# Optimization experiments

Measured on AMD Instinct MI355X. Metric: run time of the kernel, lower is better.

## Reference

```python
import jax, jax.numpy as jnp
import numpy as np

B, N, MSA, PAIR = 1, 768, 384, 128
H, SQK, PQK, SV, PV, OUT = 12, 16, 4, 16, 8, 384
EPS = 1e-8


def setup_inputs() -> dict:
    key = jax.random.key(0)
    ks = jax.random.split(key, 12)
    rn = lambda k, shape, s=1.0: jax.random.normal(k, shape, jnp.float32) * s
    return {
        "inputs_1d": rn(ks[0], (B, N, MSA)),
        "inputs_2d": rn(ks[1], (B, N, N, PAIR)),
        "rot": rn(ks[2], (B, N, 3, 3)),
        "trans": rn(ks[3], (B, N, 3)),
        "q_scalar_w": rn(ks[4], (MSA, H * SQK), 0.02),
        "q_scalar_b": jnp.zeros((H * SQK,), jnp.float32),
        "kv_scalar_w": rn(ks[5], (MSA, H * (SV + SQK)), 0.02),
        "kv_scalar_b": jnp.zeros((H * (SV + SQK),), jnp.float32),
        "q_point_w": rn(ks[6], (MSA, H * 3 * PQK), 0.02),
        "q_point_b": jnp.zeros((H * 3 * PQK,), jnp.float32),
        "kv_point_w": rn(ks[7], (MSA, H * 3 * (PQK + PV)), 0.02),
        "kv_point_b": jnp.zeros((H * 3 * (PQK + PV),), jnp.float32),
        "tpw": jnp.full((H,), 0.541323855, jnp.float32),
        "attn2d_w": rn(ks[8], (PAIR, H), 0.02),
        "attn2d_b": jnp.zeros((H,), jnp.float32),
        "out_w": rn(ks[9], (H * SV + H * PV * 4 + H * PAIR, OUT), 0.02),
        "out_b": jnp.zeros((OUT,), jnp.float32),
    }


def _ipa(inputs_1d, inputs_2d, rot, trans,
         q_scalar_w, q_scalar_b, kv_scalar_w, kv_scalar_b,
         q_point_w, q_point_b, kv_point_w, kv_point_b,
         tpw, attn2d_w, attn2d_b, out_w, out_b):
    b, n, _ = inputs_1d.shape
    # scalar q/k/v
    q_scalar = (inputs_1d @ q_scalar_w + q_scalar_b).reshape(b, n, H, SQK)
    kv_scalar = (inputs_1d @ kv_scalar_w + kv_scalar_b).reshape(b, n, H, SQK + SV)
    k_scalar, v_scalar = kv_scalar[..., :SQK], kv_scalar[..., SQK:]

    # point q/k/v: local frame -> global frame via per-residue rigid (R, t)
    def to_global(local):  # local: [b, n, 3, D]
        return jnp.einsum('bnij,bnjd->bnid', rot, local) + trans[..., None]

    qpl = (inputs_1d @ q_point_w + q_point_b).reshape(b, n, 3, H * PQK)
    # [b, H, n, PQK, 3]
    qp = to_global(qpl).reshape(b, n, 3, H, PQK).transpose(0, 3, 1, 4, 2)
    kvpl = (inputs_1d @ kv_point_w + kv_point_b).reshape(b, n, 3, H * (PQK + PV))
    kvp = to_global(kvpl).reshape(b, n, 3, H, PQK + PV).transpose(0, 3, 1, 4, 2)
    kp, vp = kvp[..., :PQK, :], kvp[..., PQK:, :]  # [b,H,n,PQK,3], [b,H,n,PV,3]

    scalar_w = (1.0 / (3.0 * SQK)) ** 0.5
    point_w = ((1.0 / (3.0 * PQK * 4.5)) ** 0.5) * jax.nn.softplus(tpw)  # [H]
    attn2d_scale = (1.0 / 3.0) ** 0.5

    # squared point distances, summed over xyz: [b, H, n, n, PQK]
    dist2 = sum(
        (qp[..., c][:, :, :, None, :] - kp[..., c][:, :, None, :, :]) ** 2
        for c in range(3))
    attn_qk_point = -0.5 * jnp.einsum('h,bhijp->bhij', point_w, dist2)

    q = scalar_w * q_scalar.transpose(0, 2, 1, 3)  # [b,H,n,SQK]
    k = k_scalar.transpose(0, 2, 1, 3)
    v = v_scalar.transpose(0, 2, 1, 3)
    attn_qk_scalar = jnp.einsum('bhid,bhjd->bhij', q, k)

    a2d = (inputs_2d @ attn2d_w + attn2d_b).transpose(0, 3, 1, 2) * attn2d_scale
    attn = jax.nn.softmax(attn_qk_scalar + attn_qk_point + a2d, axis=-1)

    result_scalar = jnp.einsum('bhij,bhjd->bhid', attn, v)
    result_scalar = result_scalar.transpose(0, 2, 1, 3).reshape(b, n, H * SV)

    rpg = jnp.einsum('bhij,bhjpc->bhipc', attn, vp)  # [b,H,n,PV,3]
    rpg = rpg.transpose(0, 2, 4, 1, 3).reshape(b, n, 3, H * PV)
    # invert point back to local frame: R^T (x - t)
    rpl = jnp.einsum('bnji,bnjd->bnid', rot, rpg - trans[..., None])  # [b,n,3,H*PV]
    pnorm = jnp.sqrt(EPS + jnp.sum(rpl ** 2, axis=2))  # [b,n,H*PV]

    a_over_2d = jnp.einsum('bhij,bijc->bihc', attn, inputs_2d).reshape(b, n, H * PAIR)

    final = jnp.concatenate(
        [result_scalar, rpl[:, :, 0], rpl[:, :, 1], rpl[:, :, 2], pnorm, a_over_2d],
        axis=-1)
    return final @ out_w + out_b


def reference(inputs_1d, inputs_2d, rot, trans,
              q_scalar_w, q_scalar_b, kv_scalar_w, kv_scalar_b,
              q_point_w, q_point_b, kv_point_w, kv_point_b,
              tpw, attn2d_w, attn2d_b, out_w, out_b):
    return _ipa(inputs_1d, inputs_2d, rot, trans,
                q_scalar_w, q_scalar_b, kv_scalar_w, kv_scalar_b,
                q_point_w, q_point_b, kv_point_w, kv_point_b,
                tpw, attn2d_w, attn2d_b, out_w, out_b)
```

## Files before the change

### kernel.cpp

```cpp
#include <hip/hip_runtime.h>
#include <hip/hip_bf16.h>

typedef unsigned int uint;
typedef unsigned short ushort;

#define SCALAR_W 0.14433756729740643f
#define PW_CONST 0.13608276348795434f
#define RSQRT3   0.57735026918962576f

#define OFF_QS    0
#define OFF_QP    147456
#define OFF_FINP  258048
#define FLOAT_END 700416
#define US_KS     1400832
#define US_VS     1548288
#define US_KP     1695744
#define US_VP     1806336
#define US_FA     2027520

__device__ __forceinline__ float blo(uint u){ return __uint_as_float(u << 16); }
__device__ __forceinline__ float bhi(uint u){ return __uint_as_float(u & 0xffff0000u); }
__device__ __forceinline__ float bf1(ushort s){ return __uint_as_float(((uint)s) << 16); }
__device__ __forceinline__ void up8(uint4 u, float* f){
  f[0]=blo(u.x); f[1]=bhi(u.x); f[2]=blo(u.y); f[3]=bhi(u.y);
  f[4]=blo(u.z); f[5]=bhi(u.z); f[6]=blo(u.w); f[7]=bhi(u.w);
}
__device__ __forceinline__ ushort f2us(float f){
  return (ushort)__bfloat16_as_ushort(__float2bfloat16(f));
}

__global__ __launch_bounds__(256) void k_proj(
    const float* __restrict__ rot, const float* __restrict__ trans,
    const float* __restrict__ qsw, const float* __restrict__ qsb,
    const float* __restrict__ kvsw, const float* __restrict__ kvsb,
    const float* __restrict__ qpw, const float* __restrict__ qpb,
    const float* __restrict__ kvpw, const float* __restrict__ kvpb,
    const float* __restrict__ in1d, float* ws){
  __shared__ float orow[1152];
  __shared__ float rotL[9], transL[3];
  const int n = blockIdx.x, t = threadIdx.x;
  const float* arow = in1d + n*384;
  if (t < 9) rotL[t] = rot[n*9+t];
  if (t >= 9 && t < 12) transL[t-9] = trans[n*3+t-9];
  #pragma unroll
  for (int r = 0; r < 3; ++r){
    int idx = t + 256*r;
    if (idx < 576){
      int o = idx*2;
      const float* w; const float* bp; int ncol, col;
      if (o < 192){ w=qsw; ncol=192; col=o; bp=qsb+col; }
      else if (o < 576){ w=kvsw; ncol=384; col=o-192; bp=kvsb+col; }
      else if (o < 720){ w=qpw; ncol=144; col=o-576; bp=qpb+col; }
      else { w=kvpw; ncol=432; col=o-720; bp=kvpb+col; }
      float2 b2 = *reinterpret_cast<const float2*>(bp);
      float a0 = b2.x, a1 = b2.y;
      const float* wp = w + col;
      #pragma unroll 4
      for (int k = 0; k < 384; ++k){
        float2 u = *reinterpret_cast<const float2*>(wp + (size_t)k*ncol);
        float av = arow[k];
        a0 += av * u.x;
        a1 += av * u.y;
      }
      orow[o] = a0; orow[o+1] = a1;
    }
  }
  __syncthreads();
  float* qs_f = ws + OFF_QS;
  float* qp_f = ws + OFF_QP;
  ushort* ws16 = reinterpret_cast<ushort*>(ws);
  ushort* kS = ws16 + US_KS;
  ushort* vS = ws16 + US_VS;
  ushort* kP = ws16 + US_KP;
  ushort* vP = ws16 + US_VP;
  if (t < 192) qs_f[n*192 + t] = orow[t] * SCALAR_W;
  for (int x = t; x < 384; x += 256){
    int h = x >> 5, d = x & 31;
    float v = orow[192 + x];
    if (d < 16) kS[(n*12 + h)*16 + d] = f2us(v);
    else        vS[(n*12 + h)*16 + (d-16)] = f2us(v);
  }
  for (int x = t; x < 144; x += 256){
    int d = x/3, c = x - 3*d;
    float g = rotL[c*3]*orow[576+d] + rotL[c*3+1]*orow[576+48+d] + rotL[c*3+2]*orow[576+96+d] + transL[c];
    qp_f[n*144 + d*3 + c] = g;
  }
  for (int x = t; x < 432; x += 256){
    int d = x/3, c = x - 3*d;
    float g = rotL[c*3]*orow[720+d] + rotL[c*3+1]*orow[720+144+d] + rotL[c*3+2]*orow[720+288+d] + transL[c];
    int h = d/12, pp = d - 12*h;
    if (pp < 4) kP[((n*12+h)*4 + pp)*3 + c] = f2us(g);
    else        vP[((n*12+h)*8 + (pp-4))*3 + c] = f2us(g);
  }
}

__global__ __launch_bounds__(256) void k_attn(
    const float* __restrict__ in2d, const float* __restrict__ rot,
    const float* __restrict__ trans, const float* __restrict__ w2d,
    const float* __restrict__ b2d, const float* __restrict__ tpw,
    float* ws){
  __shared__ __align__(16) float Ld[768*12];
  __shared__ float invL[12];
  __shared__ float pwS[12], b2S[12];
  __shared__ float rotL[9], transL[3];
  const int i = blockIdx.x, t = threadIdx.x;
  const float* qs_f = ws + OFF_QS + i*192;
  const float* qp_f = ws + OFF_QP + i*144;
  const ushort* ws16 = reinterpret_cast<const ushort*>(ws);
  const ushort* kSp = ws16 + US_KS;
  const ushort* vSp = ws16 + US_VS;
  const ushort* kPp = ws16 + US_KP;
  const ushort* vPp = ws16 + US_VP;
  if (t < 9) rotL[t] = rot[i*9+t];
  if (t >= 9 && t < 12) transL[t-9] = trans[i*3+t-9];
  if (t < 12){
    b2S[t] = b2d[t];
    pwS[t] = -0.5f * PW_CONST * log1pf(__expf(tpw[t]));
  }
  __syncthreads();
  for (int j = t; j < 768; j += 256){
    float acc12[12];
    #pragma unroll
    for (int h = 0; h < 12; ++h) acc12[h] = b2S[h];
    const float4* p2 = reinterpret_cast<const float4*>(in2d + (size_t)(i*768 + j)*128);
    #pragma unroll 4
    for (int c4 = 0; c4 < 32; ++c4){
      float4 u = p2[c4];
      const float* wr = w2d + c4*48;
      #pragma unroll
      for (int h = 0; h < 12; ++h)
        acc12[h] += u.x*wr[h] + u.y*wr[12+h] + u.z*wr[24+h] + u.w*wr[36+h];
    }
    #pragma unroll
    for (int h = 0; h < 12; ++h){
      const uint4* pk = reinterpret_cast<const uint4*>(kSp + ((size_t)j*12 + h)*16);
      uint4 a = pk[0], b = pk[1];
      float kf[16]; up8(a, kf); up8(b, kf+8);
      float qk = 0.f;
      const float* qr = qs_f + h*16;
      #pragma unroll
      for (int d = 0; d < 16; ++d) qk += qr[d] * kf[d];
      const uint2* pp = reinterpret_cast<const uint2*>(kPp + ((size_t)j*12 + h)*12);
      uint2 c0 = pp[0], c1 = pp[1], c2 = pp[2];
      float pf[12] = {blo(c0.x),bhi(c0.x),blo(c0.y),bhi(c0.y),
                      blo(c1.x),bhi(c1.x),blo(c1.y),bhi(c1.y),
                      blo(c2.x),bhi(c2.x),blo(c2.y),bhi(c2.y)};
      const float* qpr = qp_f + h*12;
      float d2 = 0.f;
      #pragma unroll
      for (int e = 0; e < 12; ++e){ float dd = qpr[e] - pf[e]; d2 += dd*dd; }
      acc12[h] = acc12[h]*RSQRT3 + qk + pwS[h]*d2;
    }
    float4* lp = reinterpret_cast<float4*>(&Ld[j*12]);
    lp[0] = make_float4(acc12[0], acc12[1], acc12[2],  acc12[3]);
    lp[1] = make_float4(acc12[4], acc12[5], acc12[6],  acc12[7]);
    lp[2] = make_float4(acc12[8], acc12[9], acc12[10], acc12[11]);
  }
  __syncthreads();
  const int wave = t >> 6, lane = t & 63;
  float invReg[3];
  #pragma unroll
  for (int s = 0; s < 3; ++s){
    int h = wave + s*4;
    float m = -1e30f;
    for (int k = 0; k < 12; ++k) m = fmaxf(m, Ld[(lane + (k<<6))*12 + h]);
    #pragma unroll
    for (int o = 32; o > 0; o >>= 1) m = fmaxf(m, __shfl_xor(m, o));
    float sum = 0.f;
    for (int k = 0; k < 12; ++k){
      int idx = (lane + (k<<6))*12 + h;
      float e = __expf(fminf(Ld[idx] - m, 0.f));
      Ld[idx] = e;
      sum += e;
    }
    #pragma unroll
    for (int o = 32; o > 0; o >>= 1) sum += __shfl_xor(sum, o);
    float inv = 1.f / sum;
    invReg[s] = inv;
    if (lane == 0) invL[h] = inv;
  }
  float* finp = ws + OFF_FINP + (size_t)i*576;
  #pragma unroll
  for (int s = 0; s < 3; ++s){
    int h = wave + s*4;
    float accS[16], accP[24];
    #pragma unroll
    for (int d = 0; d < 16; ++d) accS[d] = 0.f;
    #pragma unroll
    for (int d = 0; d < 24; ++d) accP[d] = 0.f;
    for (int it = 0; it < 12; ++it){
      int jj = lane + (it<<6);
      float e = Ld[jj*12 + h];
      const uint4* pv = reinterpret_cast<const uint4*>(vSp + ((size_t)jj*12 + h)*16);
      uint4 a = pv[0], b = pv[1];
      float vf[16]; up8(a, vf); up8(b, vf+8);
      #pragma unroll
      for (int d = 0; d < 16; ++d) accS[d] += e * vf[d];
      const uint4* pq = reinterpret_cast<const uint4*>(vPp + ((size_t)jj*12 + h)*24);
      uint4 q0 = pq[0], q1 = pq[1], q2 = pq[2];
      float pf[24]; up8(q0, pf); up8(q1, pf+8); up8(q2, pf+16);
      #pragma unroll
      for (int d = 0; d < 24; ++d) accP[d] += e * pf[d];
    }
    #pragma unroll
    for (int o2 = 32; o2 > 0; o2 >>= 1){
      #pragma unroll
      for (int d = 0; d < 16; ++d) accS[d] += __shfl_xor(accS[d], o2);
      #pragma unroll
      for (int d = 0; d < 24; ++d) accP[d] += __shfl_xor(accP[d], o2);
    }
    if (lane == 0){
      float inv = invReg[s];
      #pragma unroll
      for (int d = 0; d < 16; ++d) finp[h*16 + d] = accS[d]*inv;
      #pragma unroll
      for (int p = 0; p < 8; ++p){
        float gx = accP[p*3+0]*inv - transL[0];
        float gy = accP[p*3+1]*inv - transL[1];
        float gz = accP[p*3+2]*inv - transL[2];
        float n2 = 1e-8f;
        #pragma unroll
        for (int c = 0; c < 3; ++c){
          float r = rotL[c]*gx + rotL[3+c]*gy + rotL[6+c]*gz;
          finp[192 + c*96 + h*8 + p] = r;
          n2 += r*r;
        }
        finp[480 + h*8 + p] = sqrtf(n2);
      }
    }
  }
  __syncthreads();
  {
    const int cp = t & 63, jg = t >> 6;
    float acc[24];
    #pragma unroll
    for (int d = 0; d < 24; ++d) acc[d] = 0.f;
    const float* rowp = in2d + (size_t)i*768*128 + 2*cp;
    const int j0 = jg*192;
    for (int j = j0; j < j0 + 192; ++j){
      float2 x2 = *reinterpret_cast<const float2*>(rowp + (size_t)j*128);
      float x0 = x2.x, x1 = x2.y;
      const float4* lp = reinterpret_cast<const float4*>(&Ld[j*12]);
      float4 e0 = lp[0], e1 = lp[1], e2 = lp[2];
      acc[0] += e0.x*x0;  acc[1] += e0.x*x1;
      acc[2] += e0.y*x0;  acc[3] += e0.y*x1;
      acc[4] += e0.z*x0;  acc[5] += e0.z*x1;
      acc[6] += e0.w*x0;  acc[7] += e0.w*x1;
      acc[8] += e1.x*x0;  acc[9] += e1.x*x1;
      acc[10]+= e1.y*x0;  acc[11]+= e1.y*x1;
      acc[12]+= e1.z*x0;  acc[13]+= e1.z*x1;
      acc[14]+= e1.w*x0;  acc[15]+= e1.w*x1;
      acc[16]+= e2.x*x0;  acc[17]+= e2.x*x1;
      acc[18]+= e2.y*x0;  acc[19]+= e2.y*x1;
      acc[20]+= e2.z*x0;  acc[21]+= e2.z*x1;
      acc[22]+= e2.w*x0;  acc[23]+= e2.w*x1;
    }
    __syncthreads();
    float* LdR = Ld;
    if (jg > 0){
      #pragma unroll
      for (int d = 0; d < 24; ++d) LdR[((jg-1)*64 + cp)*25 + d] = acc[d];
    }
    __syncthreads();
    if (jg == 0){
      ushort* fa16 = reinterpret_cast<ushort*>(ws) + US_FA + (size_t)i*1536;
      float invA[12];
      #pragma unroll
      for (int h = 0; h < 12; ++h) invA[h] = invL[h];
      #pragma unroll
      for (int h = 0; h < 12; ++h){
        float a0 = acc[2*h]   + LdR[cp*25 + 2*h]   + LdR[(64+cp)*25 + 2*h]   + LdR[(128+cp)*25 + 2*h];
        float a1 = acc[2*h+1] + LdR[cp*25 + 2*h+1] + LdR[(64+cp)*25 + 2*h+1] + LdR[(128+cp)*25 + 2*h+1];
        fa16[h*128 + 2*cp]     = f2us(a0 * invA[h]);
        fa16[h*128 + 2*cp + 1] = f2us(a1 * invA[h]);
      }
    }
  }
}

__global__ __launch_bounds__(128) void k_out(const float* __restrict__ out_w,
                                             const float* __restrict__ out_b,
                                             const float* ws,
                                             float* __restrict__ out){
  __shared__ float Arow[4*2112];
  const int o = blockIdx.x*128 + threadIdx.x;
  const int ib = blockIdx.y*4;
  const ushort* ws16 = reinterpret_cast<const ushort*>(ws);
  #pragma unroll
  for (int r = 0; r < 4; ++r){
    const float* fp = ws + OFF_FINP + (size_t)(ib+r)*576;
    for (int k = threadIdx.x; k < 576; k += 128) Arow[r*2112 + k] = fp[k];
    const ushort* fa = ws16 + US_FA + (size_t)(ib+r)*1536;
    for (int k = threadIdx.x; k < 1536; k += 128) Arow[r*2112 + 576 + k] = bf1(fa[k]);
  }
  __syncthreads();
  float bc = out_b[o];
  float acc0 = bc, acc1 = bc, acc2 = bc, acc3 = bc;
  const float* wp = out_w + o;
  #pragma unroll 8
  for (int k = 0; k < 2112; ++k){
    float w = wp[(size_t)k*384];
    acc0 += Arow[k]*w; acc1 += Arow[2112+k]*w; acc2 += Arow[4224+k]*w; acc3 += Arow[6336+k]*w;
  }
  if (!(fabsf(acc0) < 1e30f)) acc0 = 1e6f;
  if (!(fabsf(acc1) < 1e30f)) acc1 = 1e6f;
  if (!(fabsf(acc2) < 1e30f)) acc2 = 1e6f;
  if (!(fabsf(acc3) < 1e30f)) acc3 = 1e6f;
  out[(ib+0)*384 + o] = acc0;
  out[(ib+1)*384 + o] = acc1;
  out[(ib+2)*384 + o] = acc2;
  out[(ib+3)*384 + o] = acc3;
}

extern "C" void kernel_launch(void* const* d_in, const int* in_sizes, int n_in,
                              void* d_out, int out_size, void* d_ws, size_t ws_size,
                              hipStream_t stream){
  const float* in1d  = (const float*)d_in[0];
  const float* in2d  = (const float*)d_in[1];
  const float* rot   = (const float*)d_in[2];
  const float* trans = (const float*)d_in[3];
  const float* qsw   = (const float*)d_in[4];
  const float* qsb   = (const float*)d_in[5];
  const float* kvsw  = (const float*)d_in[6];
  const float* kvsb  = (const float*)d_in[7];
  const float* qpw   = (const float*)d_in[8];
  const float* qpb   = (const float*)d_in[9];
  const float* kvpw  = (const float*)d_in[10];
  const float* kvpb  = (const float*)d_in[11];
  const float* tpw   = (const float*)d_in[12];
  const float* w2d   = (const float*)d_in[13];
  const float* b2d   = (const float*)d_in[14];
  const float* outw  = (const float*)d_in[15];
  const float* outb  = (const float*)d_in[16];
  float* ws = (float*)d_ws;

  k_proj<<<dim3(768), dim3(256), 0, stream>>>(rot, trans, qsw, qsb, kvsw, kvsb,
                                              qpw, qpb, kvpw, kvpb, in1d, ws);
  k_attn<<<dim3(768), dim3(256), 0, stream>>>(in2d, rot, trans, w2d, b2d, tpw, ws);
  k_out<<<dim3(3,192), dim3(128), 0, stream>>>(outw, outb, ws, (float*)d_out);
}
```

Before: 878.3 us.

## Stage pair, key and value rows through LDS with head-major packed layouts

The projection kernel now writes K scalar and K point data into one head-major packed buffer (28 bf16 per row) and stores V scalar and V point data head-major. The attention kernel loads these rows cooperatively, with coalesced wave-wide vector loads, into a per-wave LDS slice. Each lane then reads its own row from LDS. The pair-bias projection also stages in2d chunks through LDS with software prefetch. The aim is to replace strided per-lane global loads with coalesced ones, at the cost of extra LDS traffic, wave barriers and a larger shared-memory footprint that may lower occupancy.

After: 964.9 us. 9.9% more time.

```diff
diff --git a/kernel.cpp b/kernel.cpp
--- a/kernel.cpp
+++ b/kernel.cpp
@@ -11,20 +11,14 @@
 #define OFF_QS    0
 #define OFF_QP    147456
 #define OFF_FINP  258048
-#define FLOAT_END 700416
-#define US_KS     1400832
-#define US_VS     1548288
-#define US_KP     1695744
+#define US_KC     1400832
+#define US_VS     1658880
 #define US_VP     1806336
 #define US_FA     2027520
 
 __device__ __forceinline__ float blo(uint u){ return __uint_as_float(u << 16); }
 __device__ __forceinline__ float bhi(uint u){ return __uint_as_float(u & 0xffff0000u); }
 __device__ __forceinline__ float bf1(ushort s){ return __uint_as_float(((uint)s) << 16); }
-__device__ __forceinline__ void up8(uint4 u, float* f){
-  f[0]=blo(u.x); f[1]=bhi(u.x); f[2]=blo(u.y); f[3]=bhi(u.y);
-  f[4]=blo(u.z); f[5]=bhi(u.z); f[6]=blo(u.w); f[7]=bhi(u.w);
-}
 __device__ __forceinline__ ushort f2us(float f){
   return (ushort)__bfloat16_as_ushort(__float2bfloat16(f));
 }
@@ -69,16 +63,15 @@
   float* qs_f = ws + OFF_QS;
   float* qp_f = ws + OFF_QP;
   ushort* ws16 = reinterpret_cast<ushort*>(ws);
-  ushort* kS = ws16 + US_KS;
+  ushort* kC = ws16 + US_KC;
   ushort* vS = ws16 + US_VS;
-  ushort* kP = ws16 + US_KP;
   ushort* vP = ws16 + US_VP;
   if (t < 192) qs_f[n*192 + t] = orow[t] * SCALAR_W;
   for (int x = t; x < 384; x += 256){
     int h = x >> 5, d = x & 31;
     float v = orow[192 + x];
-    if (d < 16) kS[(n*12 + h)*16 + d] = f2us(v);
-    else        vS[(n*12 + h)*16 + (d-16)] = f2us(v);
+    if (d < 16) kC[((size_t)h*768 + n)*28 + d] = f2us(v);
+    else        vS[((size_t)h*768 + n)*16 + (d-16)] = f2us(v);
   }
   for (int x = t; x < 144; x += 256){
     int d = x/3, c = x - 3*d;
@@ -89,8 +82,8 @@
     int d = x/3, c = x - 3*d;
     float g = rotL[c*3]*orow[720+d] + rotL[c*3+1]*orow[720+144+d] + rotL[c*3+2]*orow[720+288+d] + transL[c];
     int h = d/12, pp = d - 12*h;
-    if (pp < 4) kP[((n*12+h)*4 + pp)*3 + c] = f2us(g);
-    else        vP[((n*12+h)*8 + (pp-4))*3 + c] = f2us(g);
+    if (pp < 4) kC[((size_t)h*768 + n)*28 + 16 + pp*3 + c] = f2us(g);
+    else        vP[((size_t)h*768 + n)*24 + (pp-4)*3 + c] = f2us(g);
   }
 }
 
@@ -100,17 +93,19 @@
     const float* __restrict__ b2d, const float* __restrict__ tpw,
     float* ws){
   __shared__ __align__(16) float Ld[768*12];
+  __shared__ __align__(16) float Sbuf[4*896];
   __shared__ float invL[12];
   __shared__ float pwS[12], b2S[12];
   __shared__ float rotL[9], transL[3];
   const int i = blockIdx.x, t = threadIdx.x;
+  const int wv = t >> 6, ln = t & 63;
   const float* qs_f = ws + OFF_QS + i*192;
   const float* qp_f = ws + OFF_QP + i*144;
   const ushort* ws16 = reinterpret_cast<const ushort*>(ws);
-  const ushort* kSp = ws16 + US_KS;
+  const ushort* kCp = ws16 + US_KC;
   const ushort* vSp = ws16 + US_VS;
-  const ushort* kPp = ws16 + US_KP;
   const ushort* vPp = ws16 + US_VP;
+  float* slice = Sbuf + wv*896;
   if (t < 9) rotL[t] = rot[i*9+t];
   if (t >= 9 && t < 12) transL[t-9] = trans[i*3+t-9];
   if (t < 12){
@@ -118,38 +113,76 @@
     pwS[t] = -0.5f * PW_CONST * log1pf(__expf(tpw[t]));
   }
   __syncthreads();
-  for (int j = t; j < 768; j += 256){
+
+  for (int jg = 0; jg < 3; ++jg){
+    const int j = jg*256 + t;
+    const int rowbase = i*768 + jg*256 + wv*64;
     float acc12[12];
     #pragma unroll
     for (int h = 0; h < 12; ++h) acc12[h] = b2S[h];
-    const float4* p2 = reinterpret_cast<const float4*>(in2d + (size_t)(i*768 + j)*128);
-    #pragma unroll 4
-    for (int c4 = 0; c4 < 32; ++c4){
-      float4 u = p2[c4];
-      const float* wr = w2d + c4*48;
-      #pragma unroll
-      for (int h = 0; h < 12; ++h)
-        acc12[h] += u.x*wr[h] + u.y*wr[12+h] + u.z*wr[24+h] + u.w*wr[36+h];
-    }
+
+    const int r0 = ln >> 1, cq = (ln & 1)*4;
+    const float* pA = in2d + (size_t)(rowbase + r0)*128 + cq;
+    const float* pB = pA + 32*128;
+    float* wr0 = slice + r0*9 + cq;
+    float* wr1 = slice + (r0+32)*9 + cq;
+    const float* rrow = slice + ln*9;
+    float4 u0 = *reinterpret_cast<const float4*>(pA);
+    float4 u1 = *reinterpret_cast<const float4*>(pB);
+    const uint4* kbase = reinterpret_cast<const uint4*>(kCp + ((size_t)jg*256 + wv*64)*28);
+    uint4 k0 = kbase[ln], k1 = kbase[ln+64], k2 = kbase[ln+128];
+    uint4 k3 = {0,0,0,0};
+    if (ln < 32) k3 = kbase[ln+192];
+    for (int cc = 0; cc < 16; ++cc){
+      wr0[0]=u0.x; wr0[1]=u0.y; wr0[2]=u0.z; wr0[3]=u0.w;
+      wr1[0]=u1.x; wr1[1]=u1.y; wr1[2]=u1.z; wr1[3]=u1.w;
+      if (cc < 15){
+        u0 = *reinterpret_cast<const float4*>(pA + (cc+1)*8);
+        u1 = *reinterpret_cast<const float4*>(pB + (cc+1)*8);
+      }
+      __builtin_amdgcn_wave_barrier();
+      #pragma unroll
+      for (int c2 = 0; c2 < 8; ++c2){
+        float x = rrow[c2];
+        const float* wp = w2d + (cc*8 + c2)*12;
+        #pragma unroll
+        for (int h = 0; h < 12; ++h) acc12[h] += x * wp[h];
+      }
+      __builtin_amdgcn_wave_barrier();
+    }
+
+    uint4* dst = reinterpret_cast<uint4*>(slice);
     #pragma unroll
     for (int h = 0; h < 12; ++h){
-      const uint4* pk = reinterpret_cast<const uint4*>(kSp + ((size_t)j*12 + h)*16);
-      uint4 a = pk[0], b = pk[1];
-      float kf[16]; up8(a, kf); up8(b, kf+8);
-      float qk = 0.f;
-      const float* qr = qs_f + h*16;
-      #pragma unroll
-      for (int d = 0; d < 16; ++d) qk += qr[d] * kf[d];
-      const uint2* pp = reinterpret_cast<const uint2*>(kPp + ((size_t)j*12 + h)*12);
-      uint2 c0 = pp[0], c1 = pp[1], c2 = pp[2];
-      float pf[12] = {blo(c0.x),bhi(c0.x),blo(c0.y),bhi(c0.y),
-                      blo(c1.x),bhi(c1.x),blo(c1.y),bhi(c1.y),
-                      blo(c2.x),bhi(c2.x),blo(c2.y),bhi(c2.y)};
+      dst[ln] = k0; dst[ln+64] = k1; dst[ln+128] = k2;
+      if (ln < 32) dst[ln+192] = k3;
+      if (h < 11){
+        const uint4* nb = kbase + (size_t)(h+1)*2688;
+        k0 = nb[ln]; k1 = nb[ln+64]; k2 = nb[ln+128];
+        if (ln < 32) k3 = nb[ln+192];
+      }
+      __builtin_amdgcn_wave_barrier();
+      const float* qr  = qs_f + h*16;
       const float* qpr = qp_f + h*12;
-      float d2 = 0.f;
-      #pragma unroll
-      for (int e = 0; e < 12; ++e){ float dd = qpr[e] - pf[e]; d2 += dd*dd; }
+      const uint2* krow = reinterpret_cast<const uint2*>(slice + ln*14);
+      float qk = 0.f, d2 = 0.f;
+      #pragma unroll
+      for (int dd = 0; dd < 4; ++dd){
+        uint2 u = krow[dd];
+        qk += qr[4*dd]   * blo(u.x) + qr[4*dd+1] * bhi(u.x)
+            + qr[4*dd+2] * blo(u.y) + qr[4*dd+3] * bhi(u.y);
+      }
+      #pragma unroll
+      for (int e2 = 0; e2 < 3; ++e2){
+        uint2 u = krow[4+e2];
+        float d0 = qpr[4*e2]   - blo(u.x);
+        float d1 = qpr[4*e2+1] - bhi(u.x);
+        float db = qpr[4*e2+2] - blo(u.y);
+        float d3 = qpr[4*e2+3] - bhi(u.y);
+        d2 += d0*d0 + d1*d1 + db*db + d3*d3;
+      }
       acc12[h] = acc12[h]*RSQRT3 + qk + pwS[h]*d2;
+      __builtin_amdgcn_wave_barrier();
     }
     float4* lp = reinterpret_cast<float4*>(&Ld[j*12]);
     lp[0] = make_float4(acc12[0], acc12[1], acc12[2],  acc12[3]);
@@ -157,50 +190,88 @@
     lp[2] = make_float4(acc12[8], acc12[9], acc12[10], acc12[11]);
   }
   __syncthreads();
-  const int wave = t >> 6, lane = t & 63;
-  float invReg[3];
+
   #pragma unroll
   for (int s = 0; s < 3; ++s){
-    int h = wave + s*4;
+    int h = wv + s*4;
     float m = -1e30f;
-    for (int k = 0; k < 12; ++k) m = fmaxf(m, Ld[(lane + (k<<6))*12 + h]);
+    for (int k = 0; k < 12; ++k) m = fmaxf(m, Ld[(ln + (k<<6))*12 + h]);
     #pragma unroll
     for (int o = 32; o > 0; o >>= 1) m = fmaxf(m, __shfl_xor(m, o));
     float sum = 0.f;
     for (int k = 0; k < 12; ++k){
-      int idx = (lane + (k<<6))*12 + h;
+      int idx = (ln + (k<<6))*12 + h;
       float e = __expf(fminf(Ld[idx] - m, 0.f));
       Ld[idx] = e;
       sum += e;
     }
     #pragma unroll
     for (int o = 32; o > 0; o >>= 1) sum += __shfl_xor(sum, o);
-    float inv = 1.f / sum;
-    invReg[s] = inv;
-    if (lane == 0) invL[h] = inv;
-  }
+    if (ln == 0) invL[h] = 1.f / sum;
+  }
+
   float* finp = ws + OFF_FINP + (size_t)i*576;
-  #pragma unroll
   for (int s = 0; s < 3; ++s){
-    int h = wave + s*4;
+    const int h = wv + s*4;
     float accS[16], accP[24];
     #pragma unroll
     for (int d = 0; d < 16; ++d) accS[d] = 0.f;
     #pragma unroll
     for (int d = 0; d < 24; ++d) accP[d] = 0.f;
-    for (int it = 0; it < 12; ++it){
-      int jj = lane + (it<<6);
-      float e = Ld[jj*12 + h];
-      const uint4* pv = reinterpret_cast<const uint4*>(vSp + ((size_t)jj*12 + h)*16);
-      uint4 a = pv[0], b = pv[1];
-      float vf[16]; up8(a, vf); up8(b, vf+8);
-      #pragma unroll
-      for (int d = 0; d < 16; ++d) accS[d] += e * vf[d];
-      const uint4* pq = reinterpret_cast<const uint4*>(vPp + ((size_t)jj*12 + h)*24);
-      uint4 q0 = pq[0], q1 = pq[1], q2 = pq[2];
-      float pf[24]; up8(q0, pf); up8(q1, pf+8); up8(q2, pf+16);
-      #pragma unroll
-      for (int d = 0; d < 24; ++d) accP[d] += e * pf[d];
+    {
+      const uint4* vb = reinterpret_cast<const uint4*>(vSp + (size_t)h*768*16);
+      uint4 a0 = vb[ln], a1 = vb[ln+64];
+      const int r = ln >> 1, c = (ln & 1)*4;
+      uint2* w0 = reinterpret_cast<uint2*>(slice + r*10 + c);
+      uint2* w1 = reinterpret_cast<uint2*>(slice + (r+32)*10 + c);
+      const uint2* vrow = reinterpret_cast<const uint2*>(slice + ln*10);
+      for (int it = 0; it < 12; ++it){
+        w0[0] = make_uint2(a0.x, a0.y); w0[1] = make_uint2(a0.z, a0.w);
+        w1[0] = make_uint2(a1.x, a1.y); w1[1] = make_uint2(a1.z, a1.w);
+        if (it < 11){
+          const uint4* nb = vb + (size_t)(it+1)*128;
+          a0 = nb[ln]; a1 = nb[ln+64];
+        }
+        __builtin_amdgcn_wave_barrier();
+        float e = Ld[((it<<6) + ln)*12 + h];
+        #pragma unroll
+        for (int dd = 0; dd < 4; ++dd){
+          uint2 u = vrow[dd];
+          accS[4*dd]   += e * blo(u.x); accS[4*dd+1] += e * bhi(u.x);
+          accS[4*dd+2] += e * blo(u.y); accS[4*dd+3] += e * bhi(u.y);
+        }
+        __builtin_amdgcn_wave_barrier();
+      }
+    }
+    {
+      const uint4* vb = reinterpret_cast<const uint4*>(vPp + (size_t)h*768*24);
+      uint4 a0 = vb[ln], a1 = vb[ln+64], a2 = vb[ln+128];
+      const int x1 = ln + 64, x2 = ln + 128;
+      const int ra = (ln*171) >> 9,  ca = (ln - 3*ra)*4;
+      const int rb = (x1*171) >> 9,  cb = (x1 - 3*rb)*4;
+      const int rc = (x2*171) >> 9,  cx = (x2 - 3*rc)*4;
+      uint2* w0 = reinterpret_cast<uint2*>(slice + ra*14 + ca);
+      uint2* w1 = reinterpret_cast<uint2*>(slice + rb*14 + cb);
+      uint2* w2 = reinterpret_cast<uint2*>(slice + rc*14 + cx);
+      const uint2* vrow = reinterpret_cast<const uint2*>(slice + ln*14);
+      for (int it = 0; it < 12; ++it){
+        w0[0] = make_uint2(a0.x, a0.y); w0[1] = make_uint2(a0.z, a0.w);
+        w1[0] = make_uint2(a1.x, a1.y); w1[1] = make_uint2(a1.z, a1.w);
+        w2[0] = make_uint2(a2.x, a2.y); w2[1] = make_uint2(a2.z, a2.w);
+        if (it < 11){
+          const uint4* nb = vb + (size_t)(it+1)*192;
+          a0 = nb[ln]; a1 = nb[ln+64]; a2 = nb[ln+128];
+        }
+        __builtin_amdgcn_wave_barrier();
+        float e = Ld[((it<<6) + ln)*12 + h];
+        #pragma unroll
+        for (int dd = 0; dd < 6; ++dd){
+          uint2 u = vrow[dd];
+          accP[4*dd]   += e * blo(u.x); accP[4*dd+1] += e * bhi(u.x);
+          accP[4*dd+2] += e * blo(u.y); accP[4*dd+3] += e * bhi(u.y);
+        }
+        __builtin_amdgcn_wave_barrier();
+      }
     }
     #pragma unroll
     for (int o2 = 32; o2 > 0; o2 >>= 1){
@@ -209,8 +280,8 @@
       #pragma unroll
       for (int d = 0; d < 24; ++d) accP[d] += __shfl_xor(accP[d], o2);
     }
-    if (lane == 0){
-      float inv = invReg[s];
+    if (ln == 0){
+      float inv = invL[h];
       #pragma unroll
       for (int d = 0; d < 16; ++d) finp[h*16 + d] = accS[d]*inv;
       #pragma unroll
@@ -221,9 +292,9 @@
         float n2 = 1e-8f;
         #pragma unroll
         for (int c = 0; c < 3; ++c){
-          float r = rotL[c]*gx + rotL[3+c]*gy + rotL[6+c]*gz;
-          finp[192 + c*96 + h*8 + p] = r;
-          n2 += r*r;
+          float rr = rotL[c]*gx + rotL[3+c]*gy + rotL[6+c]*gz;
+          finp[192 + c*96 + h*8 + p] = rr;
+          n2 += rr*rr;
         }
         finp[480 + h*8 + p] = sqrtf(n2);
       }
```

## Split attention blocks by head halves and split-K the output projection with atomics

Applied to the files above, without the earlier changes.

The attention kernel now launches two blocks per query row, each handling six heads. This halves LDS use and per-block work, and the K/V buffers are stored head-major. The output projection is split four ways along K, accumulating into the output with atomicAdd, and the bias is pre-written by the projection kernel. The trade-off is that each block pair re-reads the full in2d row, and atomics make the sum order non-deterministic. The old non-finite clamp is dropped.

Measured after the change: 752.8 us. 1.17x faster.

```diff
diff --git a/kernel.cpp b/kernel.cpp
--- a/kernel.cpp
+++ b/kernel.cpp
@@ -11,7 +11,6 @@
 #define OFF_QS    0
 #define OFF_QP    147456
 #define OFF_FINP  258048
-#define FLOAT_END 700416
 #define US_KS     1400832
 #define US_VS     1548288
 #define US_KP     1695744
@@ -35,13 +34,16 @@
     const float* __restrict__ kvsw, const float* __restrict__ kvsb,
     const float* __restrict__ qpw, const float* __restrict__ qpb,
     const float* __restrict__ kvpw, const float* __restrict__ kvpb,
-    const float* __restrict__ in1d, float* ws){
+    const float* __restrict__ in1d, const float* __restrict__ outb,
+    float* ws, float* __restrict__ out){
   __shared__ float orow[1152];
   __shared__ float rotL[9], transL[3];
   const int n = blockIdx.x, t = threadIdx.x;
-  const float* arow = in1d + n*384;
+  const float* arow = in1d + (size_t)n*384;
   if (t < 9) rotL[t] = rot[n*9+t];
   if (t >= 9 && t < 12) transL[t-9] = trans[n*3+t-9];
+  out[(size_t)n*384 + t] = outb[t];
+  if (t < 128) out[(size_t)n*384 + 256 + t] = outb[256 + t];
   #pragma unroll
   for (int r = 0; r < 3; ++r){
     int idx = t + 256*r;
@@ -77,8 +79,8 @@
   for (int x = t; x < 384; x += 256){
     int h = x >> 5, d = x & 31;
     float v = orow[192 + x];
-    if (d < 16) kS[(n*12 + h)*16 + d] = f2us(v);
-    else        vS[(n*12 + h)*16 + (d-16)] = f2us(v);
+    if (d < 16) kS[((size_t)h*768 + n)*16 + d] = f2us(v);
+    else        vS[((size_t)h*768 + n)*16 + (d-16)] = f2us(v);
   }
   for (int x = t; x < 144; x += 256){
     int d = x/3, c = x - 3*d;
@@ -89,8 +91,8 @@
     int d = x/3, c = x - 3*d;
     float g = rotL[c*3]*orow[720+d] + rotL[c*3+1]*orow[720+144+d] + rotL[c*3+2]*orow[720+288+d] + transL[c];
     int h = d/12, pp = d - 12*h;
-    if (pp < 4) kP[((n*12+h)*4 + pp)*3 + c] = f2us(g);
-    else        vP[((n*12+h)*8 + (pp-4))*3 + c] = f2us(g);
+    if (pp < 4) kP[((size_t)h*768 + n)*12 + pp*3 + c] = f2us(g);
+    else        vP[((size_t)h*768 + n)*24 + (pp-4)*3 + c] = f2us(g);
   }
 }
 
@@ -99,11 +101,12 @@
     const float* __restrict__ trans, const float* __restrict__ w2d,
     const float* __restrict__ b2d, const float* __restrict__ tpw,
     float* ws){
-  __shared__ __align__(16) float Ld[768*12];
-  __shared__ float invL[12];
-  __shared__ float pwS[12], b2S[12];
+  __shared__ __align__(16) float Ld[768*6];
+  __shared__ float invL[6];
+  __shared__ float pwS[6], b2S[6];
   __shared__ float rotL[9], transL[3];
-  const int i = blockIdx.x, t = threadIdx.x;
+  const int bid = blockIdx.x, t = threadIdx.x;
+  const int i = bid >> 1, h0 = (bid & 1)*6;
   const float* qs_f = ws + OFF_QS + i*192;
   const float* qp_f = ws + OFF_QP + i*144;
   const ushort* ws16 = reinterpret_cast<const ushort*>(ws);
@@ -113,76 +116,81 @@
   const ushort* vPp = ws16 + US_VP;
   if (t < 9) rotL[t] = rot[i*9+t];
   if (t >= 9 && t < 12) transL[t-9] = trans[i*3+t-9];
-  if (t < 12){
-    b2S[t] = b2d[t];
-    pwS[t] = -0.5f * PW_CONST * log1pf(__expf(tpw[t]));
+  if (t < 6){
+    b2S[t] = b2d[h0 + t];
+    pwS[t] = -0.5f * PW_CONST * log1pf(__expf(tpw[h0 + t]));
   }
   __syncthreads();
   for (int j = t; j < 768; j += 256){
-    float acc12[12];
-    #pragma unroll
-    for (int h = 0; h < 12; ++h) acc12[h] = b2S[h];
+    float acc6[6];
+    #pragma unroll
+    for (int h = 0; h < 6; ++h) acc6[h] = b2S[h];
     const float4* p2 = reinterpret_cast<const float4*>(in2d + (size_t)(i*768 + j)*128);
     #pragma unroll 4
     for (int c4 = 0; c4 < 32; ++c4){
       float4 u = p2[c4];
-      const float* wr = w2d + c4*48;
-      #pragma unroll
-      for (int h = 0; h < 12; ++h)
-        acc12[h] += u.x*wr[h] + u.y*wr[12+h] + u.z*wr[24+h] + u.w*wr[36+h];
-    }
-    #pragma unroll
-    for (int h = 0; h < 12; ++h){
-      const uint4* pk = reinterpret_cast<const uint4*>(kSp + ((size_t)j*12 + h)*16);
+      const float* wr = w2d + c4*48 + h0;
+      #pragma unroll
+      for (int h = 0; h < 6; ++h)
+        acc6[h] += u.x*wr[h] + u.y*wr[12+h] + u.z*wr[24+h] + u.w*wr[36+h];
+    }
+    #pragma unroll
+    for (int h = 0; h < 6; ++h){
+      const int hg = h0 + h;
+      const uint4* pk = reinterpret_cast<const uint4*>(kSp + ((size_t)hg*768 + j)*16);
       uint4 a = pk[0], b = pk[1];
       float kf[16]; up8(a, kf); up8(b, kf+8);
       float qk = 0.f;
-      const float* qr = qs_f + h*16;
+      const float* qr = qs_f + hg*16;
       #pragma unroll
       for (int d = 0; d < 16; ++d) qk += qr[d] * kf[d];
-      const uint2* pp = reinterpret_cast<const uint2*>(kPp + ((size_t)j*12 + h)*12);
+      const uint2* pp = reinterpret_cast<const uint2*>(kPp + ((size_t)hg*768 + j)*12);
       uint2 c0 = pp[0], c1 = pp[1], c2 = pp[2];
       float pf[12] = {blo(c0.x),bhi(c0.x),blo(c0.y),bhi(c0.y),
                       blo(c1.x),bhi(c1.x),blo(c1.y),bhi(c1.y),
                       blo(c2.x),bhi(c2.x),blo(c2.y),bhi(c2.y)};
-      const float* qpr = qp_f + h*12;
+      const float* qpr = qp_f + hg*12;
       float d2 = 0.f;
       #pragma unroll
       for (int e = 0; e < 12; ++e){ float dd = qpr[e] - pf[e]; d2 += dd*dd; }
-      acc12[h] = acc12[h]*RSQRT3 + qk + pwS[h]*d2;
-    }
-    float4* lp = reinterpret_cast<float4*>(&Ld[j*12]);
-    lp[0] = make_float4(acc12[0], acc12[1], acc12[2],  acc12[3]);
-    lp[1] = make_float4(acc12[4], acc12[5], acc12[6],  acc12[7]);
-    lp[2] = make_float4(acc12[8], acc12[9], acc12[10], acc12[11]);
+      acc6[h] = acc6[h]*RSQRT3 + qk + pwS[h]*d2;
+    }
+    float2* lp = reinterpret_cast<float2*>(&Ld[j*6]);
+    lp[0] = make_float2(acc6[0], acc6[1]);
+    lp[1] = make_float2(acc6[2], acc6[3]);
+    lp[2] = make_float2(acc6[4], acc6[5]);
   }
   __syncthreads();
   const int wave = t >> 6, lane = t & 63;
-  float invReg[3];
+  float invReg[2];
   #pragma unroll
-  for (int s = 0; s < 3; ++s){
+  for (int s = 0; s < 2; ++s){
     int h = wave + s*4;
-    float m = -1e30f;
-    for (int k = 0; k < 12; ++k) m = fmaxf(m, Ld[(lane + (k<<6))*12 + h]);
-    #pragma unroll
-    for (int o = 32; o > 0; o >>= 1) m = fmaxf(m, __shfl_xor(m, o));
-    float sum = 0.f;
-    for (int k = 0; k < 12; ++k){
-      int idx = (lane + (k<<6))*12 + h;
-      float e = __expf(fminf(Ld[idx] - m, 0.f));
-      Ld[idx] = e;
-      sum += e;
-    }
-    #pragma unroll
-    for (int o = 32; o > 0; o >>= 1) sum += __shfl_xor(sum, o);
-    float inv = 1.f / sum;
-    invReg[s] = inv;
-    if (lane == 0) invL[h] = inv;
+    if (h < 6){
+      float m = -1e30f;
+      for (int k = 0; k < 12; ++k) m = fmaxf(m, Ld[(lane + (k<<6))*6 + h]);
+      #pragma unroll
+      for (int o = 32; o > 0; o >>= 1) m = fmaxf(m, __shfl_xor(m, o));
+      float sum = 0.f;
+      for (int k = 0; k < 12; ++k){
+        int idx = (lane + (k<<6))*6 + h;
+        float e = __expf(fminf(Ld[idx] - m, 0.f));
+        Ld[idx] = e;
+        sum += e;
+      }
+      #pragma unroll
+      for (int o = 32; o > 0; o >>= 1) sum += __shfl_xor(sum, o);
+      float inv = 1.f / sum;
+      invReg[s] = inv;
+      if (lane == 0) invL[h] = inv;
+    }
   }
   float* finp = ws + OFF_FINP + (size_t)i*576;
   #pragma unroll
-  for (int s = 0; s < 3; ++s){
+  for (int s = 0; s < 2; ++s){
     int h = wave + s*4;
+    if (h >= 6) break;
+    const int hg = h0 + h;
     float accS[16], accP[24];
     #pragma unroll
     for (int d = 0; d < 16; ++d) accS[d] = 0.f;
@@ -190,13 +198,13 @@
     for (int d = 0; d < 24; ++d) accP[d] = 0.f;
     for (int it = 0; it < 12; ++it){
       int jj = lane + (it<<6);
-      float e = Ld[jj*12 + h];
-      const uint4* pv = reinterpret_cast<const uint4*>(vSp + ((size_t)jj*12 + h)*16);
+      float e = Ld[jj*6 + h];
+      const uint4* pv = reinterpret_cast<const uint4*>(vSp + ((size_t)hg*768 + jj)*16);
       uint4 a = pv[0], b = pv[1];
       float vf[16]; up8(a, vf); up8(b, vf+8);
       #pragma unroll
       for (int d = 0; d < 16; ++d) accS[d] += e * vf[d];
-      const uint4* pq = reinterpret_cast<const uint4*>(vPp + ((size_t)jj*12 + h)*24);
+      const uint4* pq = reinterpret_cast<const uint4*>(vPp + ((size_t)hg*768 + jj)*24);
       uint4 q0 = pq[0], q1 = pq[1], q2 = pq[2];
       float pf[24]; up8(q0, pf); up8(q1, pf+8); up8(q2, pf+16);
       #pragma unroll
@@ -212,7 +220,7 @@
     if (lane == 0){
       float inv = invReg[s];
       #pragma unroll
-      for (int d = 0; d < 16; ++d) finp[h*16 + d] = accS[d]*inv;
+      for (int d = 0; d < 16; ++d) finp[hg*16 + d] = accS[d]*inv;
       #pragma unroll
       for (int p = 0; p < 8; ++p){
         float gx = accP[p*3+0]*inv - transL[0];
@@ -222,94 +230,85 @@
         #pragma unroll
         for (int c = 0; c < 3; ++c){
           float r = rotL[c]*gx + rotL[3+c]*gy + rotL[6+c]*gz;
-          finp[192 + c*96 + h*8 + p] = r;
+          finp[192 + c*96 + hg*8 + p] = r;
           n2 += r*r;
         }
-        finp[480 + h*8 + p] = sqrtf(n2);
+        finp[480 + hg*8 + p] = sqrtf(n2);
       }
     }
   }
   __syncthreads();
   {
     const int cp = t & 63, jg = t >> 6;
-    float acc[24];
-    #pragma unroll
-    for (int d = 0; d < 24; ++d) acc[d] = 0.f;
+    float acc[12];
+    #pragma unroll
+    for (int d = 0; d < 12; ++d) acc[d] = 0.f;
     const float* rowp = in2d + (size_t)i*768*128 + 2*cp;
     const int j0 = jg*192;
     for (int j = j0; j < j0 + 192; ++j){
       float2 x2 = *reinterpret_cast<const float2*>(rowp + (size_t)j*128);
       float x0 = x2.x, x1 = x2.y;
-      const float4* lp = reinterpret_cast<const float4*>(&Ld[j*12]);
-      float4 e0 = lp[0], e1 = lp[1], e2 = lp[2];
+      const float2* lp = reinterpret_cast<const float2*>(&Ld[j*6]);
+      float2 e0 = lp[0], e1 = lp[1], e2 = lp[2];
       acc[0] += e0.x*x0;  acc[1] += e0.x*x1;
       acc[2] += e0.y*x0;  acc[3] += e0.y*x1;
-      acc[4] += e0.z*x0;  acc[5] += e0.z*x1;
-      acc[6] += e0.w*x0;  acc[7] += e0.w*x1;
-      acc[8] += e1.x*x0;  acc[9] += e1.x*x1;
-      acc[10]+= e1.y*x0;  acc[11]+= e1.y*x1;
-      acc[12]+= e1.z*x0;  acc[13]+= e1.z*x1;
-      acc[14]+= e1.w*x0;  acc[15]+= e1.w*x1;
-      acc[16]+= e2.x*x0;  acc[17]+= e2.x*x1;
-      acc[18]+= e2.y*x0;  acc[19]+= e2.y*x1;
-      acc[20]+= e2.z*x0;  acc[21]+= e2.z*x1;
-      acc[22]+= e2.w*x0;  acc[23]+= e2.w*x1;
+      acc[4] += e1.x*x0;  acc[5] += e1.x*x1;
+      acc[6] += e1.y*x0;  acc[7] += e1.y*x1;
+      acc[8] += e2.x*x0;  acc[9] += e2.x*x1;
+      acc[10]+= e2.y*x0;  acc[11]+= e2.y*x1;
     }
     __syncthreads();
     float* LdR = Ld;
     if (jg > 0){
       #pragma unroll
-      for (int d = 0; d < 24; ++d) LdR[((jg-1)*64 + cp)*25 + d] = acc[d];
+      for (int d = 0; d < 12; ++d) LdR[((jg-1)*64 + cp)*13 + d] = acc[d];
     }
     __syncthreads();
     if (jg == 0){
       ushort* fa16 = reinterpret_cast<ushort*>(ws) + US_FA + (size_t)i*1536;
-      float invA[12];
-      #pragma unroll
-      for (int h = 0; h < 12; ++h) invA[h] = invL[h];
-      #pragma unroll
-      for (int h = 0; h < 12; ++h){
-        float a0 = acc[2*h]   + LdR[cp*25 + 2*h]   + LdR[(64+cp)*25 + 2*h]   + LdR[(128+cp)*25 + 2*h];
-        float a1 = acc[2*h+1] + LdR[cp*25 + 2*h+1] + LdR[(64+cp)*25 + 2*h+1] + LdR[(128+cp)*25 + 2*h+1];
-        fa16[h*128 + 2*cp]     = f2us(a0 * invA[h]);
-        fa16[h*128 + 2*cp + 1] = f2us(a1 * invA[h]);
+      float invA[6];
+      #pragma unroll
+      for (int h = 0; h < 6; ++h) invA[h] = invL[h];
+      #pragma unroll
+      for (int h = 0; h < 6; ++h){
+        float a0 = acc[2*h]   + LdR[cp*13 + 2*h]   + LdR[(64+cp)*13 + 2*h]   + LdR[(128+cp)*13 + 2*h];
+        float a1 = acc[2*h+1] + LdR[cp*13 + 2*h+1] + LdR[(64+cp)*13 + 2*h+1] + LdR[(128+cp)*13 + 2*h+1];
+        fa16[(h0+h)*128 + 2*cp]     = f2us(a0 * invA[h]);
+        fa16[(h0+h)*128 + 2*cp + 1] = f2us(a1 * invA[h]);
       }
     }
   }
 }
 
 __global__ __launch_bounds__(128) void k_out(const float* __restrict__ out_w,
-                                             const float* __restrict__ out_b,
                                              const float* ws,
                                              float* __restrict__ out){
-  __shared__ float Arow[4*2112];
+  __shared__ float Arow[4*528];
   const int o = blockIdx.x*128 + threadIdx.x;
   const int ib = blockIdx.y*4;
+  const int k0 = blockIdx.z*528;
   const ushort* ws16 = reinterpret_cast<const ushort*>(ws);
   #pragma unroll
   for (int r = 0; r < 4; ++r){
     const float* fp = ws + OFF_FINP + (size_t)(ib+r)*576;
-    for (int k = threadIdx.x; k < 576; k += 128) Arow[r*2112 + k] = fp[k];
     const ushort* fa = ws16 + US_FA + (size_t)(ib+r)*1536;
-    for (int k = threadIdx.x; k < 1536; k += 128) Arow[r*2112 + 576 + k] = bf1(fa[k]);
-  }
-  __syncthreads();
-  float bc = out_b[o];
-  float acc0 = bc, acc1 = bc, acc2 = bc, acc3 = bc;
-  const float* wp = out_w + o;
+    for (int k = threadIdx.x; k < 528; k += 128){
+      int col = k0 + k;
+      Arow[r*528 + k] = (col < 576) ? fp[col] : bf1(fa[col - 576]);
+    }
+  }
+  __syncthreads();
+  float a0 = 0.f, a1 = 0.f, a2 = 0.f, a3 = 0.f;
+  const float* wp = out_w + (size_t)k0*384 + o;
   #pragma unroll 8
-  for (int k = 0; k < 2112; ++k){
+  for (int k = 0; k < 528; ++k){
     float w = wp[(size_t)k*384];
-    acc0 += Arow[k]*w; acc1 += Arow[2112+k]*w; acc2 += Arow[4224+k]*w; acc3 += Arow[6336+k]*w;
-  }
-  if (!(fabsf(acc0) < 1e30f)) acc0 = 1e6f;
-  if (!(fabsf(acc1) < 1e30f)) acc1 = 1e6f;
-  if (!(fabsf(acc2) < 1e30f)) acc2 = 1e6f;
-  if (!(fabsf(acc3) < 1e30f)) acc3 = 1e6f;
-  out[(ib+0)*384 + o] = acc0;
-  out[(ib+1)*384 + o] = acc1;
-  out[(ib+2)*384 + o] = acc2;
-  out[(ib+3)*384 + o] = acc3;
+    a0 += Arow[k]*w; a1 += Arow[528+k]*w; a2 += Arow[1056+k]*w; a3 += Arow[1584+k]*w;
+  }
+  atomicAdd(&out[(size_t)(ib+0)*384 + o], a0);
+  atomicAdd(&out[(size_t)(ib+1)*384 + o], a1);
+  atomicAdd(&out[(size_t)(ib+2)*384 + o], a2);
+  atomicAdd(&out[(size_t)(ib+3)*384 + o], a3);
 }
 
 extern "C" void kernel_launch(void* const* d_in, const int* in_sizes, int n_in,
@@ -335,7 +334,8 @@
   float* ws = (float*)d_ws;
 
   k_proj<<<dim3(768), dim3(256), 0, stream>>>(rot, trans, qsw, qsb, kvsw, kvsb,
-                                              qpw, qpb, kvpw, kvpb, in1d, ws);
-  k_attn<<<dim3(768), dim3(256), 0, stream>>>(in2d, rot, trans, w2d, b2d, tpw, ws);
-  k_out<<<dim3(3,192), dim3(128), 0, stream>>>(outw, outb, ws, (float*)d_out);
-}
+                                              qpw, qpb, kvpw, kvpb, in1d, outb,
+                                              ws, (float*)d_out);
+  k_attn<<<dim3(1536), dim3(256), 0, stream>>>(in2d, rot, trans, w2d, b2d, tpw, ws);
+  k_out<<<dim3(3,192,4), dim3(128), 0, stream>>>(outw, ws, (float*)d_out);
+}
```
